# Kernel tuning notes

Measured on AMD Instinct MI355X. Metric: run time of the kernel, lower is better.

The kernel has to match this reference:

```python
import jax, jax.numpy as jnp
import numpy as np

B, T, IN = 8, 1000, 80
CONV = 256
CCEP = 222            # ltv_out_channels
FFT_SIZE = 1024
HOP = 256
WIN = 2 * HOP         # 512
PAD = (FFT_SIZE - CCEP) // 2   # 401
NFFT = 2048


def _conv1d_same(x, W, b, groups):
    # x: (B,T,C); W: (O, C//groups, 3); equivalent to torch Conv1d pad=2 then [1:-1]
    y = jax.lax.conv_general_dilated(
        jnp.transpose(x, (0, 2, 1)), W, (1,), [(1, 1)],
        feature_group_count=groups,
        dimension_numbers=('NCH', 'OIH', 'NCH'))
    return jnp.transpose(y, (0, 2, 1)) + b


def _forward(x, z, W1, b1, W2, b2, W3, b3, W4, b4):
    Bx, Tx, _ = x.shape
    # ---- ConvLayers ----
    h = jax.nn.relu(_conv1d_same(x, W1, b1, 1))
    h = jax.nn.relu(_conv1d_same(h, W2, b2, 8))
    h = jax.nn.relu(_conv1d_same(h, W3, b3, 8))
    ccep = _conv1d_same(h, W4, b4, 1)            # (B,T,222)
    q = jnp.arange(1, CCEP // 2 + 1, dtype=x.dtype)
    quef = jnp.concatenate([q[::-1], q])          # [111..1,1..111]
    ccep = ccep / quef
    # ---- ccep -> impulse (log-magnitude cepstrum -> minimum-ish phase impulse) ----
    c = jnp.pad(ccep, ((0, 0), (0, 0), (PAD, PAD)))           # (B,T,1024)
    Y = jnp.fft.fft(c, n=FFT_SIZE, axis=-1)
    mag = jnp.power(10.0, Y.real)
    imp = jnp.fft.ifft(mag * jnp.exp(1j * Y.imag), n=FFT_SIZE, axis=-1).real  # (B,T,1024)
    # ---- time-varying impulse convolution (cross-correlation per frame) ----
    L = z.shape[-1]
    zz = z.reshape(Bx, 1, L)
    zp = jnp.pad(zz, ((0, 0), (0, 0), (WIN // 2 - 1, WIN // 2)))
    starts = jnp.arange(Tx) * HOP
    frames = zp[:, :, starts[:, None] + jnp.arange(WIN)]       # (B,1,T,512)
    fp = jnp.pad(frames, ((0, 0), (0, 0), (0, 0), (FFT_SIZE // 2 - 1, FFT_SIZE // 2)))  # len 1535
    # corr[s] = sum_k fp[s+k] * imp[k], s in [0,512); linear corr via zero-padded FFT
    Fz = jnp.fft.rfft(fp, n=NFFT, axis=-1)                     # (B,1,T,NFFT//2+1)
    Fy = jnp.fft.rfft(imp, n=NFFT, axis=-1)[:, None]           # (B,1,T,NFFT//2+1)
    corr = jnp.fft.irfft(Fz * jnp.conj(Fy), n=NFFT, axis=-1)[..., :WIN]  # (B,1,T,512)
    # ---- overlap-add ----
    n = jnp.arange(WIN, dtype=x.dtype)
    win = 0.5 * (1.0 - jnp.cos(2.0 * jnp.pi * n / WIN))        # periodic hann, win_norm=1
    zw = corr * win
    l, r = zw[..., :HOP], zw[..., HOP:]
    out = l + jnp.roll(r, 1, axis=2)
    return out.reshape(Bx, 1, Tx * HOP)


def setup_inputs() -> dict:
    key = jax.random.key(0)
    ks = jax.random.split(key, 12)
    x = jax.random.normal(ks[0], (B, T, IN), dtype=jnp.float32)
    z = jax.random.normal(ks[1], (B, 1, T * HOP), dtype=jnp.float32)
    def w(k, o, i, kk, scale):
        return jax.random.normal(k, (o, i, kk), dtype=jnp.float32) * (scale / np.sqrt(i * kk))
    W1 = w(ks[2], CONV, IN, 3, 1.0)
    b1 = jnp.zeros((CONV,), jnp.float32)
    W2 = w(ks[3], CONV, CONV // 8, 3, 1.0)
    b2 = jnp.zeros((CONV,), jnp.float32)
    W3 = w(ks[4], CONV, CONV // 8, 3, 1.0)
    b3 = jnp.zeros((CONV,), jnp.float32)
    W4 = w(ks[5], CCEP, CONV, 3, 0.01)   # small scale keeps 10**(.) well-conditioned
    b4 = jnp.zeros((CCEP,), jnp.float32)
    return {"x": x, "z": z, "W1": W1, "b1": b1, "W2": W2, "b2": b2,
            "W3": W3, "b3": b3, "W4": W4, "b4": b4}


def reference(x, z, W1, b1, W2, b2, W3, b3, W4, b4):
    return _forward(x, z, W1, b1, W2, b2, W3, b3, W4, b4)
```

## Files before the change

kernel.cpp:

```cpp
#include <hip/hip_runtime.h>
#include <hip/hip_bf16.h>

#define T_LEN 1000
#define B_N 8
#define IN_CH 80
#define CONV_CH 256
#define CCEP_N 222

typedef short s8v __attribute__((ext_vector_type(8)));
typedef _Float16 h8v __attribute__((ext_vector_type(8)));
typedef float f16v __attribute__((ext_vector_type(16)));

#define TWO_PI 6.28318530717958647692f

__global__ __launch_bounds__(256) void k_prep(
    const float* __restrict__ W1, const float* __restrict__ W2,
    const float* __restrict__ W3, const float* __restrict__ W4,
    _Float16* __restrict__ W1p, _Float16* __restrict__ W2p,
    _Float16* __restrict__ W3p,
    __hip_bfloat16* __restrict__ Wc, float2* __restrict__ twTab,
    float* __restrict__ winTab) {
  const int bid = blockIdx.x, tid = threadIdx.x;
  if (bid < 288) {
    int e = bid * 256 + tid;
    int kloc = e & 31, n = (e >> 5) & 255, chg = e >> 13;
    int k = chg * 32 + kloc;
    int kappa = k / 96, i = k - kappa * 96;
    W1p[e] = (i < IN_CH) ? (_Float16)W1[n * 240 + i * 3 + kappa] : (_Float16)0.f;
  } else if (bid < 384) {
    int e = (bid - 288) * 256 + tid;
    int kloc = e & 31, n = (e >> 5) & 255, chg = e >> 13;
    int k = chg * 32 + kloc;
    int kappa = k >> 5, iloc = k & 31;
    W2p[e] = (_Float16)W2[n * 96 + iloc * 3 + kappa];
  } else if (bid < 480) {
    int e = (bid - 384) * 256 + tid;
    int kloc = e & 31, n = (e >> 5) & 255, chg = e >> 13;
    int k = chg * 32 + kloc;
    int kappa = k >> 5, iloc = k & 31;
    W3p[e] = (_Float16)W3[n * 96 + iloc * 3 + kappa];
  } else if (bid < 1248) {
    int e = (bid - 480) * 256 + tid;
    int kloc = e & 31, n = (e >> 5) & 255, chg = e >> 13;
    int kp = chg * 32 + kloc;
    int kappa = kp >> 8, i = kp & 255;
    float v = 0.f;
    if (n < CCEP_N) {
      float invq = 1.f / (float)((n < 111) ? (111 - n) : (n - 110));
      v = W4[n * 768 + i * 3 + kappa] * invq;
    }
    Wc[e] = __float2bfloat16(v);
  } else {
    int e = (bid - 1248) * 256 + tid;
    if (e < 1020) {
      int Q, off;
      if (e < 768)       { Q = 256; off = 0; }
      else if (e < 960)  { Q = 64;  off = 768; }
      else if (e < 1008) { Q = 16;  off = 960; }
      else               { Q = 4;   off = 1008; }
      int rem = e - off;
      int r = rem / Q, pos = rem - r * Q;
      float ang = (TWO_PI * (float)((r + 1) * pos)) / (float)(4 * Q);
      float s, c;
      sincosf(ang, &s, &c);
      twTab[e] = make_float2(c, s);
    } else if (e < 1532) {
      int n = e - 1020;
      winTab[n] = (0.5f - 0.5f * cosf(TWO_PI * (float)n / 512.f)) * (1.f / 1024.f);
    }
  }
}

#define XP2 112
#define HP2 144
#define BP2 48

__global__ __launch_bounds__(256) void k_convfused(
    const float* __restrict__ x,
    const _Float16* __restrict__ W1p, const float* __restrict__ b1,
    const _Float16* __restrict__ W2p, const float* __restrict__ b2,
    const _Float16* __restrict__ W3p, const float* __restrict__ b3,
    __hip_bfloat16* __restrict__ out) {
  const int mb = blockIdx.x, b = blockIdx.y, z = blockIdx.z;
  const int t0 = mb * 32;
  const int tid = threadIdx.x;
  const int w = tid >> 6, lane = tid & 63;
  const int lm = lane & 31, half = lane >> 5;
  const int n0loc = w * 32;
  const int c = z * 128 + n0loc + lm;

  __shared__ _Float16 xs[38 * XP2];
  __shared__ _Float16 h1s[36 * HP2];
  __shared__ _Float16 h2s[34 * HP2];
  __shared__ _Float16 Bs[2][128 * BP2];

  for (int e = tid; e < 38 * 96; e += 256) {
    int rr = e / 96, cc = e - rr * 96;
    int t = t0 - 3 + rr;
    float v = (cc < IN_CH && t >= 0 && t < T_LEN)
                  ? x[(b * T_LEN + t) * IN_CH + cc] : 0.f;
    xs[rr * XP2 + cc] = (_Float16)v;
  }
  {
    const _Float16* src = W1p + z * 4096;
    for (int e = tid; e < 512; e += 256) {
      int nl = e >> 2, c4 = e & 3;
      *(uint4*)(Bs[0] + nl * BP2 + c4 * 8) = *(const uint4*)(src + nl * 32 + c4 * 8);
    }
  }
  __syncthreads();

  {
    f16v a0 = {}, a1 = {};
    for (int chg = 0; chg < 9; ++chg) {
      const int p = chg & 1;
      if (chg + 1 < 9) {
        const _Float16* src = W1p + (size_t)(chg + 1) * 8192 + z * 4096;
        for (int e = tid; e < 512; e += 256) {
          int nl = e >> 2, c4 = e & 3;
          *(uint4*)(Bs[p ^ 1] + nl * BP2 + c4 * 8) = *(const uint4*)(src + nl * 32 + c4 * 8);
        }
      }
#pragma unroll
      for (int s = 0; s < 2; ++s) {
        const int c16 = chg * 2 + s;
        const int kappa = c16 / 6;
        const int icol = (c16 - kappa * 6) * 16;
        h8v bf = *(const h8v*)(Bs[p] + (n0loc + lm) * BP2 + s * 16 + half * 8);
        h8v aa0 = *(const h8v*)(xs + (lm + kappa) * XP2 + icol + half * 8);
        h8v aa1 = *(const h8v*)(xs + (lm + kappa + 4) * XP2 + icol + half * 8);
        a0 = __builtin_amdgcn_mfma_f32_32x32x16_f16(aa0, bf, a0, 0, 0, 0);
        a1 = __builtin_amdgcn_mfma_f32_32x32x16_f16(aa1, bf, a1, 0, 0, 0);
      }
      __syncthreads();
    }
    const float bv = b1[c];
#pragma unroll
    for (int reg = 0; reg < 16; ++reg) {
      int row = (reg & 3) + 8 * (reg >> 2) + 4 * half;
      {
        int t = t0 - 2 + row;
        float v = (t >= 0 && t < T_LEN) ? fmaxf(a0[reg] + bv, 0.f) : 0.f;
        h1s[row * HP2 + n0loc + lm] = (_Float16)v;
      }
      if (row >= 28) {
        int t = t0 + 2 + row;
        float v = (t >= 0 && t < T_LEN) ? fmaxf(a1[reg] + bv, 0.f) : 0.f;
        h1s[(row + 4) * HP2 + n0loc + lm] = (_Float16)v;
      }
    }
  }
  {
    const _Float16* src = W2p + z * 4096;
    for (int e = tid; e < 512; e += 256) {
      int nl = e >> 2, c4 = e & 3;
      *(uint4*)(Bs[0] + nl * BP2 + c4 * 8) = *(const uint4*)(src + nl * 32 + c4 * 8);
    }
  }
  __syncthreads();

  {
    f16v a0 = {}, a1 = {};
    for (int chg = 0; chg < 3; ++chg) {
      const int p = chg & 1;
      if (chg + 1 < 3) {
        const _Float16* src = W2p + (size_t)(chg + 1) * 8192 + z * 4096;
        for (int e = tid; e < 512; e += 256) {
          int nl = e >> 2, c4 = e & 3;
          *(uint4*)(Bs[p ^ 1] + nl * BP2 + c4 * 8) = *(const uint4*)(src + nl * 32 + c4 * 8);
        }
      }
#pragma unroll
      for (int s = 0; s < 2; ++s) {
        const int c16 = chg * 2 + s;
        const int kappa = c16 >> 1;
        const int icol = n0loc + (c16 & 1) * 16;
        h8v bf = *(const h8v*)(Bs[p] + (n0loc + lm) * BP2 + s * 16 + half * 8);
        h8v aa0 = *(const h8v*)(h1s + (lm + kappa) * HP2 + icol + half * 8);
        h8v aa1 = *(const h8v*)(h1s + (lm + kappa + 2) * HP2 + icol + half * 8);
        a0 = __builtin_amdgcn_mfma_f32_32x32x16_f16(aa0, bf, a0, 0, 0, 0);
        a1 = __builtin_amdgcn_mfma_f32_32x32x16_f16(aa1, bf, a1, 0, 0, 0);
      }
      __syncthreads();
    }
    const float bv = b2[c];
#pragma unroll
    for (int reg = 0; reg < 16; ++reg) {
      int row = (reg & 3) + 8 * (reg >> 2) + 4 * half;
      {
        int t = t0 - 1 + row;
        float v = (t >= 0 && t < T_LEN) ? fmaxf(a0[reg] + bv, 0.f) : 0.f;
        h2s[row * HP2 + n0loc + lm] = (_Float16)v;
      }
      if (row >= 30) {
        int t = t0 + 1 + row;
        float v = (t >= 0 && t < T_LEN) ? fmaxf(a1[reg] + bv, 0.f) : 0.f;
        h2s[(row + 2) * HP2 + n0loc + lm] = (_Float16)v;
      }
    }
  }
  {
    const _Float16* src = W3p + z * 4096;
    for (int e = tid; e < 512; e += 256) {
      int nl = e >> 2, c4 = e & 3;
      *(uint4*)(Bs[0] + nl * BP2 + c4 * 8) = *(const uint4*)(src + nl * 32 + c4 * 8);
    }
  }
  __syncthreads();

  {
    f16v a0 = {};
    for (int chg = 0; chg < 3; ++chg) {
      const int p = chg & 1;
      if (chg + 1 < 3) {
        const _Float16* src = W3p + (size_t)(chg + 1) * 8192 + z * 4096;
        for (int e = tid; e < 512; e += 256) {
          int nl = e >> 2, c4 = e & 3;
          *(uint4*)(Bs[p ^ 1] + nl * BP2 + c4 * 8) = *(const uint4*)(src + nl * 32 + c4 * 8);
        }
      }
#pragma unroll
      for (int s = 0; s < 2; ++s) {
        const int c16 = chg * 2 + s;
        const int kappa = c16 >> 1;
        const int icol = n0loc + (c16 & 1) * 16;
        h8v bf = *(const h8v*)(Bs[p] + (n0loc + lm) * BP2 + s * 16 + half * 8);
        h8v aa = *(const h8v*)(h2s + (lm + kappa) * HP2 + icol + half * 8);
        a0 = __builtin_amdgcn_mfma_f32_32x32x16_f16(aa, bf, a0, 0, 0, 0);
      }
      __syncthreads();
    }
    const float bv = b3[c];
#pragma unroll
    for (int reg = 0; reg < 16; ++reg) {
      int row = (reg & 3) + 8 * (reg >> 2) + 4 * half;
      int t = t0 + row;
      if (t < T_LEN)
        out[(size_t)(b * T_LEN + t) * CONV_CH + c] =
            __float2bfloat16(fmaxf(a0[reg] + bv, 0.f));
    }
  }
}

#define APITCH 264
#define BPITCH 40
#define PSTRIDE 1792000
__global__ __launch_bounds__(256) void k_conv4m(
    const __hip_bfloat16* __restrict__ h3, const __hip_bfloat16* __restrict__ Wc,
    const float* __restrict__ bias, float* __restrict__ Pbase) {
  const int mb = blockIdx.x, b = blockIdx.y, ks = blockIdx.z;
  float* __restrict__ P = Pbase + (size_t)ks * PSTRIDE;
  const int t0 = mb * 64;
  const int tid = threadIdx.x;
  const int w = tid >> 6, lane = tid & 63;
  const int wm = w >> 1, wn = w & 1;
  const int lm = lane & 31, half = lane >> 5;

  __shared__ short h3s[67 * APITCH];
  __shared__ short Bs[2][256 * BPITCH];

  const ushort* h3u = (const ushort*)h3;
  for (int g = tid; g < 67 * 64; g += 256) {
    int rr = g >> 6, c4 = g & 63;
    int t = t0 + rr - 1;
    uint2 v = make_uint2(0u, 0u);
    if (t >= 0 && t < T_LEN)
      v = *(const uint2*)(h3u + (b * T_LEN + t) * CONV_CH + c4 * 4);
    *(uint2*)(h3s + rr * APITCH + c4 * 4) = v;
  }

  const ushort* Wu = (const ushort*)(Wc) + (size_t)(ks * 6) * 8192;
#pragma unroll
  for (int it = 0; it < 4; ++it) {
    int idx = (it * 256 + tid) * 8;
    uint4 v = *(const uint4*)(Wu + idx);
    int n = idx >> 5, kloc = idx & 31;
    *(uint4*)(Bs[0] + n * BPITCH + kloc) = v;
  }
  __syncthreads();

  f16v acc0 = {}, acc1 = {}, acc2 = {}, acc3 = {};

  for (int ch = 0; ch < 6; ++ch) {
    const int p = ch & 1;
    if (ch < 5) {
      const ushort* src = Wu + (ch + 1) * 8192;
#pragma unroll
      for (int it = 0; it < 4; ++it) {
        int idx = (it * 256 + tid) * 8;
        uint4 v = *(const uint4*)(src + idx);
        int n = idx >> 5, kloc = idx & 31;
        *(uint4*)(Bs[p ^ 1] + n * BPITCH + kloc) = v;
      }
    }
#pragma unroll
    for (int s = 0; s < 2; ++s) {
      int k0 = ks * 192 + ch * 32 + s * 16;
      int kappa = k0 >> 8, i0 = k0 & 255;
      s8v a = *(const s8v*)(h3s + (wm * 32 + lm + kappa) * APITCH + i0 + half * 8);
      const short* bp = Bs[p] + (wn * 128 + lm) * BPITCH + s * 16 + half * 8;
      s8v b0 = *(const s8v*)(bp);
      s8v b1 = *(const s8v*)(bp + 32 * BPITCH);
      s8v b2 = *(const s8v*)(bp + 64 * BPITCH);
      s8v b3 = *(const s8v*)(bp + 96 * BPITCH);
      acc0 = __builtin_amdgcn_mfma_f32_32x32x16_bf16(a, b0, acc0, 0, 0, 0);
      acc1 = __builtin_amdgcn_mfma_f32_32x32x16_bf16(a, b1, acc1, 0, 0, 0);
      acc2 = __builtin_amdgcn_mfma_f32_32x32x16_bf16(a, b2, acc2, 0, 0, 0);
      acc3 = __builtin_amdgcn_mfma_f32_32x32x16_bf16(a, b3, acc3, 0, 0, 0);
    }
    __syncthreads();
  }

  const int col = lm;
#pragma unroll
  for (int nt = 0; nt < 4; ++nt) {
    int c = wn * 128 + nt * 32 + col;
    if (c >= CCEP_N) continue;
    float bq = 0.f;
    if (ks == 0) {
      float invq = 1.f / (float)((c < 111) ? (111 - c) : (c - 110));
      bq = bias[c] * invq;
    }
    const f16v* A = (nt == 0) ? &acc0 : (nt == 1) ? &acc1 : (nt == 2) ? &acc2 : &acc3;
#pragma unroll
    for (int reg = 0; reg < 16; ++reg) {
      int row = (reg & 3) + 8 * (reg >> 2) + 4 * half;
      int t = t0 + wm * 32 + row;
      if (t < T_LEN)
        P[(size_t)(b * T_LEN + t) * 224 + c] = (*A)[reg] + bq;
    }
  }
}

__device__ __forceinline__ float2 cmul(float2 a, float2 b) {
  return make_float2(fmaf(a.x, b.x, -(a.y * b.y)), fmaf(a.x, b.y, a.y * b.x));
}
__device__ __forceinline__ float2 cadd(float2 a, float2 b) { return make_float2(a.x + b.x, a.y + b.y); }
__device__ __forceinline__ float2 csub(float2 a, float2 b) { return make_float2(a.x - b.x, a.y - b.y); }

#define LIDX(i) ((i) + ((i) >> 2))

template <int Q, int OFF>
__device__ __forceinline__ void fwd_stage2(float2* __restrict__ A,
    float2* __restrict__ B, const float2* __restrict__ Tw, int j) {
  const int pos = j & (Q - 1);
  const int base = ((j - pos) << 2) + pos;
  float2 e1 = Tw[OFF + pos], e2 = Tw[OFF + Q + pos], e3 = Tw[OFF + 2 * Q + pos];
  const float2 w1 = make_float2(e1.x, -e1.y);
  const float2 w2 = make_float2(e2.x, -e2.y);
  const float2 w3 = make_float2(e3.x, -e3.y);
#pragma unroll
  for (int arr = 0; arr < 2; ++arr) {
    float2* X = arr ? B : A;
    float2 a = X[LIDX(base)], b = X[LIDX(base + Q)];
    float2 cc = X[LIDX(base + 2 * Q)], d = X[LIDX(base + 3 * Q)];
    float2 t0 = cadd(a, cc), t1 = csub(a, cc), t2 = cadd(b, d), bd = csub(b, d);
    float2 t3 = make_float2(bd.y, -bd.x);
    X[LIDX(base)]         = cadd(t0, t2);
    X[LIDX(base + Q)]     = cmul(cadd(t1, t3), w1);
    X[LIDX(base + 2 * Q)] = cmul(csub(t0, t2), w2);
    X[LIDX(base + 3 * Q)] = cmul(csub(t1, t3), w3);
  }
}

template <int Q, int OFF>
__device__ __forceinline__ void inv_stage_t(float2* __restrict__ X,
    const float2* __restrict__ Tw, int j) {
  const int pos = j & (Q - 1);
  const int base = ((j - pos) << 2) + pos;
  const float2 w1 = Tw[OFF + pos];
  const float2 w2 = Tw[OFF + Q + pos];
  const float2 w3 = Tw[OFF + 2 * Q + pos];
  float2 a = X[LIDX(base)];
  float2 b = cmul(X[LIDX(base + Q)], w1);
  float2 cc = cmul(X[LIDX(base + 2 * Q)], w2);
  float2 d = cmul(X[LIDX(base + 3 * Q)], w3);
  float2 t0 = cadd(a, cc), t1 = csub(a, cc), t2 = cadd(b, d), bd = csub(b, d);
  float2 t3 = make_float2(-bd.y, bd.x);
  X[LIDX(base)]         = cadd(t0, t2);
  X[LIDX(base + Q)]     = cadd(t1, t3);
  X[LIDX(base + 2 * Q)] = csub(t0, t2);
  X[LIDX(base + 3 * Q)] = csub(t1, t3);
}

__device__ __forceinline__ int rev4d(int v) {
  return ((v & 3) << 6) | (((v >> 2) & 3) << 4) | (((v >> 4) & 3) << 2) | ((v >> 6) & 3);
}

__global__ __launch_bounds__(256) void k_fft(const float* __restrict__ Pb,
    const float* __restrict__ z, const float2* __restrict__ twg,
    const float* __restrict__ wing, float* __restrict__ out,
    float* __restrict__ sbl, float* __restrict__ sbr) {
  const int u = blockIdx.x, b = blockIdx.y;
  const int tA = 2 * u, tB = tA + 1;
  const int btA = b * T_LEN + tA, btB = btA + 1;
  const int j = threadIdx.x;
  __shared__ float2 WlA[1280];
  __shared__ float2 WlB[1280];
  __shared__ float2 Tws[1020];
  for (int e = j; e < 1020; e += 256) Tws[e] = twg[e];

  const float* zb = z + b * 256000;
  float f0A = 0.f, fS, f1B = 0.f;
  {
    int zi0 = tA * 256 + j - 255;
    f0A = (zi0 >= 0) ? zb[zi0] : 0.f;
    fS = zb[tA * 256 + j + 1];
    int zi2 = tB * 256 + j + 1;
    f1B = (zi2 < 256000) ? zb[zi2] : 0.f;
  }
  float c1A = 0.f, c2A = 0.f, c1B = 0.f, c2B = 0.f;
  if (j >= 145) {
    int mA = btA * 224 + (j - 145), mB = btB * 224 + (j - 145);
    c1A = (Pb[mA] + Pb[mA + PSTRIDE]) + (Pb[mA + 2 * PSTRIDE] + Pb[mA + 3 * PSTRIDE]);
    c1B = (Pb[mB] + Pb[mB + PSTRIDE]) + (Pb[mB + 2 * PSTRIDE] + Pb[mB + 3 * PSTRIDE]);
  }
  if (j < 111) {
    int mA = btA * 224 + (j + 111), mB = btB * 224 + (j + 111);
    c2A = (Pb[mA] + Pb[mA + PSTRIDE]) + (Pb[mA + 2 * PSTRIDE] + Pb[mA + 3 * PSTRIDE]);
    c2B = (Pb[mB] + Pb[mB + PSTRIDE]) + (Pb[mB + 2 * PSTRIDE] + Pb[mB + 3 * PSTRIDE]);
  }
  __syncthreads();

  {
    float2 e1 = Tws[j], e2 = Tws[256 + j], e3 = Tws[512 + j];
    const float2 w1 = make_float2(e1.x, -e1.y);
    const float2 w2 = make_float2(e2.x, -e2.y);
    const float2 w3 = make_float2(e3.x, -e3.y);
    {
      float2 t0 = make_float2(c2A, f0A);
      float2 t1 = make_float2(-c2A, f0A);
      float2 t2 = make_float2(c1A, fS);
      float2 t3 = make_float2(fS, -c1A);
      WlA[LIDX(j)]       = cadd(t0, t2);
      WlA[LIDX(j + 256)] = cmul(cadd(t1, t3), w1);
      WlA[LIDX(j + 512)] = cmul(csub(t0, t2), w2);
      WlA[LIDX(j + 768)] = cmul(csub(t1, t3), w3);
    }
    {
      float2 t0 = make_float2(c2B, fS);
      float2 t1 = make_float2(-c2B, fS);
      float2 t2 = make_float2(c1B, f1B);
      float2 t3 = make_float2(f1B, -c1B);
      WlB[LIDX(j)]       = cadd(t0, t2);
      WlB[LIDX(j + 256)] = cmul(cadd(t1, t3), w1);
      WlB[LIDX(j + 512)] = cmul(csub(t0, t2), w2);
      WlB[LIDX(j + 768)] = cmul(csub(t1, t3), w3);
    }
  }
  __syncthreads();

  fwd_stage2<64, 768>(WlA, WlB, Tws, j);  __syncthreads();
  fwd_stage2<16, 960>(WlA, WlB, Tws, j);  __syncthreads();
  fwd_stage2<4, 1008>(WlA, WlB, Tws, j);  __syncthreads();

  const int base = 4 * j;
  float2 XA[4], XB[4];
  {
    float2 u0 = WlA[LIDX(base)], u1 = WlA[LIDX(base + 1)];
    float2 u2 = WlA[LIDX(base + 2)], u3 = WlA[LIDX(base + 3)];
    float2 t0 = cadd(u0, u2), t1 = csub(u0, u2), t2 = cadd(u1, u3), bd = csub(u1, u3);
    float2 t3 = make_float2(bd.y, -bd.x);
    XA[0] = cadd(t0, t2); XA[1] = cadd(t1, t3); XA[2] = csub(t0, t2); XA[3] = csub(t1, t3);
  }
  {
    float2 u0 = WlB[LIDX(base)], u1 = WlB[LIDX(base + 1)];
    float2 u2 = WlB[LIDX(base + 2)], u3 = WlB[LIDX(base + 3)];
    float2 t0 = cadd(u0, u2), t1 = csub(u0, u2), t2 = cadd(u1, u3), bd = csub(u1, u3);
    float2 t3 = make_float2(bd.y, -bd.x);
    XB[0] = cadd(t0, t2); XB[1] = cadd(t1, t3); XB[2] = csub(t0, t2); XB[3] = csub(t1, t3);
  }
#pragma unroll
  for (int q = 0; q < 4; ++q) { WlA[LIDX(base + q)] = XA[q]; WlB[LIDX(base + q)] = XB[q]; }
  __syncthreads();

  const int r0 = rev4d(j);
  const bool self0 = (r0 == 0);
  const int jp = self0 ? 0 : rev4d((256 - r0) & 255);
  float2 PA[4], PB[4];
#pragma unroll
  for (int q = 0; q < 4; ++q) { PA[q] = WlA[LIDX(4 * jp + q)]; PB[q] = WlB[LIDX(4 * jp + q)]; }
  float2 Z[4];
#pragma unroll
  for (int q = 0; q < 4; ++q) {
    float2 SA, SB;
    {
      float2 A = XA[q];
      float2 Bc = self0 ? PA[(4 - q) & 3] : PA[3 - q];
      float2 Y = make_float2(0.5f * (A.x + Bc.x), 0.5f * (A.y - Bc.y));
      float2 F = make_float2(0.5f * (A.y + Bc.y), -0.5f * (A.x - Bc.x));
      float mag = __expf(Y.x * 2.30258509299404568402f);
      float sy, cy;
      __sincosf(Y.y, &sy, &cy);
      float gr = mag * cy, gi = mag * sy;
      SA = make_float2(fmaf(F.x, gr, F.y * gi), fmaf(F.x, gi, -(F.y * gr)));
    }
    {
      float2 A = XB[q];
      float2 Bc = self0 ? PB[(4 - q) & 3] : PB[3 - q];
      float2 Y = make_float2(0.5f * (A.x + Bc.x), 0.5f * (A.y - Bc.y));
      float2 F = make_float2(0.5f * (A.y + Bc.y), -0.5f * (A.x - Bc.x));
      float mag = __expf(Y.x * 2.30258509299404568402f);
      float sy, cy;
      __sincosf(Y.y, &sy, &cy);
      float gr = mag * cy, gi = mag * sy;
      SB = make_float2(fmaf(F.x, gr, F.y * gi), fmaf(F.x, gi, -(F.y * gr)));
    }
    Z[q] = make_float2(SA.x - SB.y, SA.y + SB.x);
  }
  __syncthreads();

  {
    float2 t0 = cadd(Z[0], Z[2]), t1 = csub(Z[0], Z[2]), t2 = cadd(Z[1], Z[3]), bd = csub(Z[1], Z[3]);
    float2 t3 = make_float2(-bd.y, bd.x);
    WlA[LIDX(base)]     = cadd(t0, t2);
    WlA[LIDX(base + 1)] = cadd(t1, t3);
    WlA[LIDX(base + 2)] = csub(t0, t2);
    WlA[LIDX(base + 3)] = csub(t1, t3);
  }
  __syncthreads();

  inv_stage_t<4, 1008>(WlA, Tws, j);  __syncthreads();
  inv_stage_t<16, 960>(WlA, Tws, j);  __syncthreads();
  inv_stage_t<64, 768>(WlA, Tws, j);  __syncthreads();

  {
    float2 w1 = Tws[j], w2 = Tws[256 + j], w3 = Tws[512 + j];
    float2 a = WlA[LIDX(j)];
    float2 bb = cmul(WlA[LIDX(j + 256)], w1);
    float2 cc = cmul(WlA[LIDX(j + 512)], w2);
    float2 d = cmul(WlA[LIDX(j + 768)], w3);
    float2 t0 = cadd(a, cc), t1 = csub(a, cc), t2 = cadd(bb, d), bd = csub(bb, d);
    float2 t3 = make_float2(-bd.y, bd.x);
    float2 Cj    = cadd(t0, t2);
    float2 Cj256 = cadd(t1, t3);
    int n1 = 511 - j, n2 = 255 - j;
    float wn1 = wing[n1], wn2 = wing[n2];
    float vA_l = Cj256.x * wn2;
    float vAB  = Cj.x * wn1 + Cj256.y * wn2;
    float vB_r = Cj.y * wn1;
    out[(b * T_LEN + tB) * 256 + n2] = vAB;
    int su = (b * 500 + u) * 256 + n2;
    sbl[su] = vA_l;
    sbr[su] = vB_r;
  }
}

__global__ __launch_bounds__(256) void k_even(const float* __restrict__ sbl,
    const float* __restrict__ sbr, float* __restrict__ out) {
  int idx = blockIdx.x * 256 + threadIdx.x;
  int n = idx & 255;
  int bu = idx >> 8;
  int u = bu % 500, b = bu / 500;
  int up = (u == 0) ? 499 : u - 1;
  out[(b * T_LEN + 2 * u) * 256 + n] = sbl[idx] + sbr[(b * 500 + up) * 256 + n];
}

extern "C" void kernel_launch(void* const* d_in, const int* in_sizes, int n_in,
                              void* d_out, int out_size, void* d_ws, size_t ws_size,
                              hipStream_t stream) {
  const float* x  = (const float*)d_in[0];
  const float* z  = (const float*)d_in[1];
  const float* W1 = (const float*)d_in[2];
  const float* b1 = (const float*)d_in[3];
  const float* W2 = (const float*)d_in[4];
  const float* b2 = (const float*)d_in[5];
  const float* W3 = (const float*)d_in[6];
  const float* b3 = (const float*)d_in[7];
  const float* W4 = (const float*)d_in[8];
  const float* b4 = (const float*)d_in[9];

  float* ws   = (float*)d_ws;
  __hip_bfloat16* h3bf = (__hip_bfloat16*)ws;
  float* Pb   = ws + 1024000;
  float* sbl  = ws + 8192000;
  float* sbr  = ws + 9216000;
  _Float16* W1p = (_Float16*)(ws + 10240000);
  _Float16* W2p = (_Float16*)(ws + 10301440);
  _Float16* W3p = (_Float16*)(ws + 10326016);
  __hip_bfloat16* Wc = (__hip_bfloat16*)(ws + 10350592);
  float2* twTab = (float2*)(ws + 10448896);
  float* winTab = ws + 10450944;
  float* out = (float*)d_out;

  dim3 blk(256);
  k_prep<<<1254, blk, 0, stream>>>(W1, W2, W3, W4, W1p, W2p, W3p,
                                   Wc, twTab, winTab);

  dim3 gc(32, B_N, 2);
  k_convfused<<<gc, blk, 0, stream>>>(x, W1p, b1, W2p, b2, W3p, b3, h3bf);
  dim3 g4(16, B_N, 4);
  k_conv4m<<<g4, blk, 0, stream>>>(h3bf, Wc, b4, Pb);
  dim3 gf(T_LEN / 2, B_N);
  k_fft<<<gf, blk, 0, stream>>>(Pb, z, twTab, winTab, out, sbl, sbr);
  k_even<<<4000, blk, 0, stream>>>(sbl, sbr, out);
}
```

Before: 150.4 us.

## Drop split-K in conv4 GEMM and overlap W4/twiddle prep with conv blocks

The final conv GEMM no longer splits K into four partial outputs. Each block now covers 32 timesteps across the full K=768 and writes a single P buffer, so the FFT kernel loads one value per coefficient instead of summing four partials. The W4 weight packing and the twiddle/window tables move out of k_prep into an extra z-slice of the fused conv kernel, so they run alongside the first conv layers. In exchange, conv4 has longer per-block K loops and fewer accumulators per wave.

Result: slower. 154.0 us (+2.4%).

```diff
diff --git a/kernel.cpp b/kernel.cpp
--- a/kernel.cpp
+++ b/kernel.cpp
@@ -15,11 +15,9 @@
 
 __global__ __launch_bounds__(256) void k_prep(
     const float* __restrict__ W1, const float* __restrict__ W2,
-    const float* __restrict__ W3, const float* __restrict__ W4,
+    const float* __restrict__ W3,
     _Float16* __restrict__ W1p, _Float16* __restrict__ W2p,
-    _Float16* __restrict__ W3p,
-    __hip_bfloat16* __restrict__ Wc, float2* __restrict__ twTab,
-    float* __restrict__ winTab) {
+    _Float16* __restrict__ W3p) {
   const int bid = blockIdx.x, tid = threadIdx.x;
   if (bid < 288) {
     int e = bid * 256 + tid;
@@ -33,41 +31,12 @@
     int k = chg * 32 + kloc;
     int kappa = k >> 5, iloc = k & 31;
     W2p[e] = (_Float16)W2[n * 96 + iloc * 3 + kappa];
-  } else if (bid < 480) {
+  } else {
     int e = (bid - 384) * 256 + tid;
     int kloc = e & 31, n = (e >> 5) & 255, chg = e >> 13;
     int k = chg * 32 + kloc;
     int kappa = k >> 5, iloc = k & 31;
     W3p[e] = (_Float16)W3[n * 96 + iloc * 3 + kappa];
-  } else if (bid < 1248) {
-    int e = (bid - 480) * 256 + tid;
-    int kloc = e & 31, n = (e >> 5) & 255, chg = e >> 13;
-    int kp = chg * 32 + kloc;
-    int kappa = kp >> 8, i = kp & 255;
-    float v = 0.f;
-    if (n < CCEP_N) {
-      float invq = 1.f / (float)((n < 111) ? (111 - n) : (n - 110));
-      v = W4[n * 768 + i * 3 + kappa] * invq;
-    }
-    Wc[e] = __float2bfloat16(v);
-  } else {
-    int e = (bid - 1248) * 256 + tid;
-    if (e < 1020) {
-      int Q, off;
-      if (e < 768)       { Q = 256; off = 0; }
-      else if (e < 960)  { Q = 64;  off = 768; }
-      else if (e < 1008) { Q = 16;  off = 960; }
-      else               { Q = 4;   off = 1008; }
-      int rem = e - off;
-      int r = rem / Q, pos = rem - r * Q;
-      float ang = (TWO_PI * (float)((r + 1) * pos)) / (float)(4 * Q);
-      float s, c;
-      sincosf(ang, &s, &c);
-      twTab[e] = make_float2(c, s);
-    } else if (e < 1532) {
-      int n = e - 1020;
-      winTab[n] = (0.5f - 0.5f * cosf(TWO_PI * (float)n / 512.f)) * (1.f / 1024.f);
-    }
   }
 }
 
@@ -80,10 +49,49 @@
     const _Float16* __restrict__ W1p, const float* __restrict__ b1,
     const _Float16* __restrict__ W2p, const float* __restrict__ b2,
     const _Float16* __restrict__ W3p, const float* __restrict__ b3,
-    __hip_bfloat16* __restrict__ out) {
+    __hip_bfloat16* __restrict__ out,
+    const float* __restrict__ W4, __hip_bfloat16* __restrict__ Wc,
+    float2* __restrict__ twTab, float* __restrict__ winTab) {
+  const int tid = threadIdx.x;
+
+  if (blockIdx.z == 2) {
+    int blk = blockIdx.y * 32 + blockIdx.x;
+    for (int e = blk * 256 + tid; e < 196608 + 1532; e += 65536) {
+      if (e < 196608) {
+        int kloc = e & 31, n = (e >> 5) & 255, chg = e >> 13;
+        int kp = chg * 32 + kloc;
+        int kappa = kp >> 8, i = kp & 255;
+        float v = 0.f;
+        if (n < CCEP_N) {
+          float invq = 1.f / (float)((n < 111) ? (111 - n) : (n - 110));
+          v = W4[n * 768 + i * 3 + kappa] * invq;
+        }
+        Wc[e] = __float2bfloat16(v);
+      } else {
+        int e2 = e - 196608;
+        if (e2 < 1020) {
+          int Q, off;
+          if (e2 < 768)       { Q = 256; off = 0; }
+          else if (e2 < 960)  { Q = 64;  off = 768; }
+          else if (e2 < 1008) { Q = 16;  off = 960; }
+          else                { Q = 4;   off = 1008; }
+          int rem = e2 - off;
+          int r = rem / Q, pos = rem - r * Q;
+          float ang = (TWO_PI * (float)((r + 1) * pos)) / (float)(4 * Q);
+          float s, c;
+          sincosf(ang, &s, &c);
+          twTab[e2] = make_float2(c, s);
+        } else if (e2 < 1532) {
+          int n = e2 - 1020;
+          winTab[n] = (0.5f - 0.5f * cosf(TWO_PI * (float)n / 512.f)) * (1.f / 1024.f);
+        }
+      }
+    }
+    return;
+  }
+
   const int mb = blockIdx.x, b = blockIdx.y, z = blockIdx.z;
   const int t0 = mb * 32;
-  const int tid = threadIdx.x;
   const int w = tid >> 6, lane = tid & 63;
   const int lm = lane & 31, half = lane >> 5;
   const int n0loc = w * 32;
@@ -242,34 +250,31 @@
   }
 }
 
-#define APITCH 264
+#define AP4 264
 #define BPITCH 40
-#define PSTRIDE 1792000
 __global__ __launch_bounds__(256) void k_conv4m(
     const __hip_bfloat16* __restrict__ h3, const __hip_bfloat16* __restrict__ Wc,
-    const float* __restrict__ bias, float* __restrict__ Pbase) {
-  const int mb = blockIdx.x, b = blockIdx.y, ks = blockIdx.z;
-  float* __restrict__ P = Pbase + (size_t)ks * PSTRIDE;
-  const int t0 = mb * 64;
+    const float* __restrict__ bias, float* __restrict__ P) {
+  const int mb = blockIdx.x, b = blockIdx.y;
+  const int t0 = mb * 32;
   const int tid = threadIdx.x;
   const int w = tid >> 6, lane = tid & 63;
-  const int wm = w >> 1, wn = w & 1;
   const int lm = lane & 31, half = lane >> 5;
 
-  __shared__ short h3s[67 * APITCH];
+  __shared__ short h3s[34 * AP4];
   __shared__ short Bs[2][256 * BPITCH];
 
   const ushort* h3u = (const ushort*)h3;
-  for (int g = tid; g < 67 * 64; g += 256) {
+  for (int g = tid; g < 34 * 64; g += 256) {
     int rr = g >> 6, c4 = g & 63;
     int t = t0 + rr - 1;
     uint2 v = make_uint2(0u, 0u);
     if (t >= 0 && t < T_LEN)
       v = *(const uint2*)(h3u + (b * T_LEN + t) * CONV_CH + c4 * 4);
-    *(uint2*)(h3s + rr * APITCH + c4 * 4) = v;
-  }
-
-  const ushort* Wu = (const ushort*)(Wc) + (size_t)(ks * 6) * 8192;
+    *(uint2*)(h3s + rr * AP4 + c4 * 4) = v;
+  }
+
+  const ushort* Wu = (const ushort*)Wc;
 #pragma unroll
   for (int it = 0; it < 4; ++it) {
     int idx = (it * 256 + tid) * 8;
@@ -279,12 +284,12 @@
   }
   __syncthreads();
 
-  f16v acc0 = {}, acc1 = {}, acc2 = {}, acc3 = {};
-
-  for (int ch = 0; ch < 6; ++ch) {
+  f16v acc0 = {}, acc1 = {};
+
+  for (int ch = 0; ch < 24; ++ch) {
     const int p = ch & 1;
-    if (ch < 5) {
-      const ushort* src = Wu + (ch + 1) * 8192;
+    if (ch < 23) {
+      const ushort* src = Wu + (size_t)(ch + 1) * 8192;
 #pragma unroll
       for (int it = 0; it < 4; ++it) {
         int idx = (it * 256 + tid) * 8;
@@ -295,37 +300,29 @@
     }
 #pragma unroll
     for (int s = 0; s < 2; ++s) {
-      int k0 = ks * 192 + ch * 32 + s * 16;
+      int k0 = ch * 32 + s * 16;
       int kappa = k0 >> 8, i0 = k0 & 255;
-      s8v a = *(const s8v*)(h3s + (wm * 32 + lm + kappa) * APITCH + i0 + half * 8);
-      const short* bp = Bs[p] + (wn * 128 + lm) * BPITCH + s * 16 + half * 8;
+      s8v a = *(const s8v*)(h3s + (lm + kappa) * AP4 + i0 + half * 8);
+      const short* bp = Bs[p] + (w * 64 + lm) * BPITCH + s * 16 + half * 8;
       s8v b0 = *(const s8v*)(bp);
       s8v b1 = *(const s8v*)(bp + 32 * BPITCH);
-      s8v b2 = *(const s8v*)(bp + 64 * BPITCH);
-      s8v b3 = *(const s8v*)(bp + 96 * BPITCH);
       acc0 = __builtin_amdgcn_mfma_f32_32x32x16_bf16(a, b0, acc0, 0, 0, 0);
       acc1 = __builtin_amdgcn_mfma_f32_32x32x16_bf16(a, b1, acc1, 0, 0, 0);
-      acc2 = __builtin_amdgcn_mfma_f32_32x32x16_bf16(a, b2, acc2, 0, 0, 0);
-      acc3 = __builtin_amdgcn_mfma_f32_32x32x16_bf16(a, b3, acc3, 0, 0, 0);
     }
     __syncthreads();
   }
 
-  const int col = lm;
-#pragma unroll
-  for (int nt = 0; nt < 4; ++nt) {
-    int c = wn * 128 + nt * 32 + col;
+#pragma unroll
+  for (int nt = 0; nt < 2; ++nt) {
+    int c = w * 64 + nt * 32 + lm;
     if (c >= CCEP_N) continue;
-    float bq = 0.f;
-    if (ks == 0) {
-      float invq = 1.f / (float)((c < 111) ? (111 - c) : (c - 110));
-      bq = bias[c] * invq;
-    }
-    const f16v* A = (nt == 0) ? &acc0 : (nt == 1) ? &acc1 : (nt == 2) ? &acc2 : &acc3;
+    float invq = 1.f / (float)((c < 111) ? (111 - c) : (c - 110));
+    float bq = bias[c] * invq;
+    const f16v* A = nt ? &acc1 : &acc0;
 #pragma unroll
     for (int reg = 0; reg < 16; ++reg) {
       int row = (reg & 3) + 8 * (reg >> 2) + 4 * half;
-      int t = t0 + wm * 32 + row;
+      int t = t0 + row;
       if (t < T_LEN)
         P[(size_t)(b * T_LEN + t) * 224 + c] = (*A)[reg] + bq;
     }
@@ -412,13 +409,13 @@
   float c1A = 0.f, c2A = 0.f, c1B = 0.f, c2B = 0.f;
   if (j >= 145) {
     int mA = btA * 224 + (j - 145), mB = btB * 224 + (j - 145);
-    c1A = (Pb[mA] + Pb[mA + PSTRIDE]) + (Pb[mA + 2 * PSTRIDE] + Pb[mA + 3 * PSTRIDE]);
-    c1B = (Pb[mB] + Pb[mB + PSTRIDE]) + (Pb[mB + 2 * PSTRIDE] + Pb[mB + 3 * PSTRIDE]);
+    c1A = Pb[mA];
+    c1B = Pb[mB];
   }
   if (j < 111) {
     int mA = btA * 224 + (j + 111), mB = btB * 224 + (j + 111);
-    c2A = (Pb[mA] + Pb[mA + PSTRIDE]) + (Pb[mA + 2 * PSTRIDE] + Pb[mA + 3 * PSTRIDE]);
-    c2B = (Pb[mB] + Pb[mB + PSTRIDE]) + (Pb[mB + 2 * PSTRIDE] + Pb[mB + 3 * PSTRIDE]);
+    c2A = Pb[mA];
+    c2B = Pb[mB];
   }
   __syncthreads();
 
@@ -584,12 +581,12 @@
   float* out = (float*)d_out;
 
   dim3 blk(256);
-  k_prep<<<1254, blk, 0, stream>>>(W1, W2, W3, W4, W1p, W2p, W3p,
-                                   Wc, twTab, winTab);
-
-  dim3 gc(32, B_N, 2);
-  k_convfused<<<gc, blk, 0, stream>>>(x, W1p, b1, W2p, b2, W3p, b3, h3bf);
-  dim3 g4(16, B_N, 4);
+  k_prep<<<480, blk, 0, stream>>>(W1, W2, W3, W1p, W2p, W3p);
+
+  dim3 gc(32, B_N, 3);
+  k_convfused<<<gc, blk, 0, stream>>>(x, W1p, b1, W2p, b2, W3p, b3, h3bf,
+                                      W4, Wc, twTab, winTab);
+  dim3 g4(32, B_N);
   k_conv4m<<<g4, blk, 0, stream>>>(h3bf, Wc, b4, Pb);
   dim3 gf(T_LEN / 2, B_N);
   k_fft<<<gf, blk, 0, stream>>>(Pb, z, twTab, winTab, out, sbl, sbr);
```
